# Performance work log

Measured on AMD Instinct MI355X. Metric: run time of the kernel, lower is better.

The kernel has to match this reference:

```python
import jax, jax.numpy as jnp
import numpy as np

K = 7          # kernel_size from init
PAD = (K - 1) // 2
EPS = 1e-8


def _local_std(x):
    """Per-pixel std of the zero-padded KxK x C neighborhood, matching
    torch: unfold(pad=3) -> mean over dim=1 (C*K*K) -> sqrt(mean(d^2)+eps).
    Computed with box-filter convolutions instead of materializing the
    49x-blown-up unfold tensor.
    Returns [B, H*W].
    """
    B, C, H, W = x.shape
    n = C * K * K  # fixed divisor (zero padding counts toward the mean)
    ones = jnp.ones((1, C, K, K), x.dtype)  # OIHW: sums over channels + window
    s = jax.lax.conv_general_dilated(x, ones, (1, 1), [(PAD, PAD), (PAD, PAD)])      # [B,1,H,W]
    s2 = jax.lax.conv_general_dilated(x * x, ones, (1, 1), [(PAD, PAD), (PAD, PAD)])  # [B,1,H,W]
    mu = s / n
    var = s2 / n - mu * mu  # E[x^2] - mu^2 == mean((x-mu)^2)
    return jnp.sqrt(var + EPS).reshape(B, H * W)


def _smooth_l1_mean(a, b):
    d = a - b
    ad = jnp.abs(d)
    per = jnp.where(ad < 1.0, 0.5 * d * d, ad - 0.5)
    return jnp.mean(per)


def setup_inputs() -> dict:
    key = jax.random.key(0)
    k1, k2 = jax.random.split(key)
    shape = (16, 3, 512, 512)
    pred_moire = jax.random.normal(k1, shape, dtype=jnp.float32)
    moire = jax.random.normal(k2, shape, dtype=jnp.float32)
    return {"pred_moire": pred_moire, "moire": moire}


def reference(pred_moire, moire):
    std_pred = _local_std(pred_moire)  # [B, H*W]
    std_tgt = _local_std(moire)        # [B, H*W]
    return _smooth_l1_mean(std_pred, std_tgt)  # scalar
```

## Files before the change

### kernel.cpp

```cpp
#include <hip/hip_runtime.h>


typedef float f32x4 __attribute__((ext_vector_type(4)));

#define K     7
#define PAD   3
#define TSX   64
#define TSY   32
#define HR    (TSY + K - 1)
#define LDSW  64
#define NT    256
#define NTASK (2 * HR * 8)

#define LOADQ(dst, ptr, OFF)                                        \
    asm volatile("global_load_dwordx4 %0, %1, off offset:" OFF      \
                 : "=v"(dst) : "v"(ptr))

#define WAITV(N) do {                                               \
    asm volatile("s_waitcnt vmcnt(" #N ")" ::: "memory");           \
    __builtin_amdgcn_sched_barrier(0);                              \
} while (0)

__global__ __launch_bounds__(NT, 2) void dist_loss_kernel(
    const float* __restrict__ pred,
    const float* __restrict__ tgt,
    float* __restrict__ out)
{
    constexpr int   C = 3, H = 512, W = 512;
    constexpr float INV_N     = 1.0f / (C * K * K);
    constexpr float INV_TOTAL = 1.0f / (16.0f * 512.0f * 512.0f);

    __shared__ float sh_s[2][HR][LDSW];
    __shared__ float sh_q[2][HR][LDSW];

    const int    tid  = threadIdx.x;
    const int    tx0  = blockIdx.x * TSX;
    const int    ty0  = blockIdx.y * TSY;
    const int    b    = blockIdx.z;
    const size_t plane = (size_t)H * W;

    const float* base0 = pred + (size_t)b * C * plane;
    const float* base1 = tgt  + (size_t)b * C * plane;

    float* shs = &sh_s[0][0][0];
    float* shq = &sh_q[0][0][0];

    #define DECL_SLOT(S)                                                     \
        const float *rB0_##S, *rB1_##S, *rB2_##S,                            \
                    *pA0_##S, *pA1_##S, *pA2_##S,                            \
                    *pE0_##S, *pE1_##S, *pE2_##S;                            \
        f32x4 qA0_##S, qB0_##S, qD0_##S, qE0_##S,                            \
              qA1_##S, qB1_##S, qD1_##S, qE1_##S,                            \
              qA2_##S, qB2_##S, qD2_##S, qE2_##S;                            \
        float m_##S, mL_##S, mR_##S; int idx_##S;

    #define SETUP(S, t) do {                                                 \
        const int which = ((t) >= HR * 8) ? 1 : 0;                           \
        const int tt    = (t) - which * (HR * 8);                            \
        const int row   = tt >> 3, cg = tt & 7;                              \
        const int gy    = ty0 - PAD + row;                                   \
        m_##S  = ((unsigned)gy < (unsigned)H) ? 1.f : 0.f;                   \
        const int gyc = min(max(gy, 0), H - 1);                              \
        const int gx0 = tx0 + (cg << 3);                                     \
        mL_##S = (gx0 > 0)   ? 1.f : 0.f;                                    \
        mR_##S = (gx0 < 504) ? 1.f : 0.f;                                    \
        const float* base = which ? base1 : base0;                           \
        rB0_##S = base + (size_t)gyc * W + gx0;                              \
        rB1_##S = rB0_##S + plane;                                           \
        rB2_##S = rB1_##S + plane;                                           \
        pA0_##S = rB0_##S + ((gx0 > 0)   ? -4 : 0);                          \
        pA1_##S = pA0_##S + plane;                                           \
        pA2_##S = pA1_##S + plane;                                           \
        pE0_##S = rB0_##S + ((gx0 < 504) ?  4 : 0);     \
        pE1_##S = pE0_##S + plane;                                           \
        pE2_##S = pE1_##S + plane;                                           \
        idx_##S = (which * HR + row) * LDSW + (cg << 3);                     \
    } while (0)

    #define ISSUE(S) do {                                                    \
        LOADQ(qA0_##S, pA0_##S, "0");  LOADQ(qB0_##S, rB0_##S, "0");         \
        LOADQ(qD0_##S, rB0_##S, "16"); LOADQ(qE0_##S, pE0_##S, "16");        \
        LOADQ(qA1_##S, pA1_##S, "0");  LOADQ(qB1_##S, rB1_##S, "0");         \
        LOADQ(qD1_##S, rB1_##S, "16"); LOADQ(qE1_##S, pE1_##S, "16");        \
        LOADQ(qA2_##S, pA2_##S, "0");  LOADQ(qB2_##S, rB2_##S, "0");         \
        LOADQ(qD2_##S, rB2_##S, "16"); LOADQ(qE2_##S, pE2_##S, "16");        \
    } while (0)

    #define CONSUME(S) do {                                                  \
        f32x4 tl = qA0_##S + qA1_##S + qA2_##S;                              \
        f32x4 ta = qB0_##S + qB1_##S + qB2_##S;                              \
        f32x4 tb = qD0_##S + qD1_##S + qD2_##S;                              \
        f32x4 tr = qE0_##S + qE1_##S + qE2_##S;                              \
        f32x4 ul = qA0_##S*qA0_##S + qA1_##S*qA1_##S + qA2_##S*qA2_##S;      \
        f32x4 ua = qB0_##S*qB0_##S + qB1_##S*qB1_##S + qB2_##S*qB2_##S;      \
        f32x4 ub = qD0_##S*qD0_##S + qD1_##S*qD1_##S + qD2_##S*qD2_##S;      \
        f32x4 ur = qE0_##S*qE0_##S + qE1_##S*qE1_##S + qE2_##S*qE2_##S;      \
        tl[1] *= mL_##S; tl[2] *= mL_##S; tl[3] *= mL_##S;                   \
        ul[1] *= mL_##S; ul[2] *= mL_##S; ul[3] *= mL_##S;                   \
        tr[0] *= mR_##S; tr[1] *= mR_##S; tr[2] *= mR_##S;                   \
        ur[0] *= mR_##S; ur[1] *= mR_##S; ur[2] *= mR_##S;                   \
        float h0 = tl[1]+tl[2]+tl[3]+ta[0]+ta[1]+ta[2]+ta[3];                \
        float h1 = h0 - tl[1] + tb[0];                                       \
        float h2 = h1 - tl[2] + tb[1];                                       \
        float h3 = h2 - tl[3] + tb[2];                                       \
        float h4 = h3 - ta[0] + tb[3];                                       \
        float h5 = h4 - ta[1] + tr[0];                                       \
        float h6 = h5 - ta[2] + tr[1];                                       \
        float h7 = h6 - ta[3] + tr[2];                                       \
        float g0 = ul[1]+ul[2]+ul[3]+ua[0]+ua[1]+ua[2]+ua[3];                \
        float g1 = g0 - ul[1] + ub[0];                                       \
        float g2 = g1 - ul[2] + ub[1];                                       \
        float g3 = g2 - ul[3] + ub[2];                                       \
        float g4 = g3 - ua[0] + ub[3];                                       \
        float g5 = g4 - ua[1] + ur[0];                                       \
        float g6 = g5 - ua[2] + ur[1];                                       \
        float g7 = g6 - ua[3] + ur[2];                                       \
        const float mm = m_##S;                                              \
        *(f32x4*)&shs[idx_##S]     = (f32x4){h0*mm, h1*mm, h2*mm, h3*mm};    \
        *(f32x4*)&shs[idx_##S + 4] = (f32x4){h4*mm, h5*mm, h6*mm, h7*mm};    \
        *(f32x4*)&shq[idx_##S]     = (f32x4){g0*mm, g1*mm, g2*mm, g3*mm};    \
        *(f32x4*)&shq[idx_##S + 4] = (f32x4){g4*mm, g5*mm, g6*mm, g7*mm};    \
    } while (0)

    DECL_SLOT(0);
    DECL_SLOT(1);
    const int t0 = tid;
    const int t1 = tid + NT;
    const int t2 = min(tid + 2 * NT, NTASK - 1);

    SETUP(0, t0); ISSUE(0);
    SETUP(1, t1); ISSUE(1);
    WAITV(12);
    CONSUME(0);
    SETUP(0, t2); ISSUE(0);
    WAITV(12);
    CONSUME(1);
    WAITV(0);
    CONSUME(0);

    __syncthreads();

    float acc = 0.0f;
    {
        const int rp = tid >> 4;
        const int x  = (tid & 15) << 2;

        f32x4 pA, pB;

        #define STD4(Sv, Qv, D) do {                                         \
            _Pragma("unroll")                                                \
            for (int c_ = 0; c_ < 4; ++c_) {                                 \
                float mu_ = (Sv)[c_] * INV_N;                                \
                (D)[c_] = sqrtf(fmaf(-mu_, mu_, (Qv)[c_] * INV_N) + 1e-8f);  \
            }                                                                \
        } while (0)
        #define SL1(a, bb) do {                                              \
            float d_  = (a) - (bb);                                          \
            float ad_ = fabsf(d_);                                           \
            acc += (ad_ < 1.0f) ? 0.5f * d_ * d_ : (ad_ - 0.5f);             \
        } while (0)

        #pragma unroll
        for (int w = 0; w < 2; ++w) {
            f32x4 S = (f32x4){0.f, 0.f, 0.f, 0.f};
            f32x4 Q = (f32x4){0.f, 0.f, 0.f, 0.f};
            #pragma unroll
            for (int k = 0; k < K; ++k) {
                S += *(const f32x4*)&sh_s[w][2 * rp + k][x];
                Q += *(const f32x4*)&sh_q[w][2 * rp + k][x];
            }
            f32x4 S2 = S - *(const f32x4*)&sh_s[w][2 * rp][x]
                         + *(const f32x4*)&sh_s[w][2 * rp + 7][x];
            f32x4 Q2 = Q - *(const f32x4*)&sh_q[w][2 * rp][x]
                         + *(const f32x4*)&sh_q[w][2 * rp + 7][x];

            if (w == 0) {
                STD4(S, Q, pA);
                STD4(S2, Q2, pB);
            } else {
                f32x4 sA, sB;
                STD4(S, Q, sA);
                STD4(S2, Q2, sB);
                SL1(pA[0], sA[0]); SL1(pA[1], sA[1]);
                SL1(pA[2], sA[2]); SL1(pA[3], sA[3]);
                SL1(pB[0], sB[0]); SL1(pB[1], sB[1]);
                SL1(pB[2], sB[2]); SL1(pB[3], sB[3]);
            }
        }
        #undef STD4
        #undef SL1
    }

    #pragma unroll
    for (int off = 32; off > 0; off >>= 1)
        acc += __shfl_down(acc, off, 64);

    __shared__ float wave_sums[NT / 64];
    if ((tid & 63) == 0) wave_sums[tid >> 6] = acc;
    __syncthreads();
    if (tid == 0) {
        float s = 0.0f;
        #pragma unroll
        for (int w = 0; w < NT / 64; ++w) s += wave_sums[w];
        atomicAdd(out, s * INV_TOTAL);
    }
}

extern "C" void kernel_launch(void* const* d_in, const int* in_sizes, int n_in,
                              void* d_out, int out_size, void* d_ws, size_t ws_size,
                              hipStream_t stream) {
    const float* pred = (const float*)d_in[0];
    const float* tgt  = (const float*)d_in[1];
    float* out = (float*)d_out;

    hipMemsetAsync(out, 0, sizeof(float), stream);

    dim3 grid(512 / TSX, 512 / TSY, 16);
    dist_loss_kernel<<<grid, NT, 0, stream>>>(pred, tgt, out);
}
```

Before: 130.2 us.

## Process four row tiles per block with double-buffered LDS and overlapped loads

Each block now walks four vertical tiles instead of one. It keeps three load slots in flight and prefetches the next tile's global loads while the current tile's vertical box-sum and loss phase runs out of a second LDS buffer. The intent is to hide global-memory latency behind compute and to cut the per-block launch and reduction overhead, since the grid shrinks fourfold. In exchange it uses more dynamic LDS (two buffers, near the two-blocks-per-CU limit) and more registers, and the grid becomes small enough to leave little slack for load balancing.

```diff
diff --git a/kernel.cpp b/kernel.cpp
--- a/kernel.cpp
+++ b/kernel.cpp
@@ -11,6 +11,7 @@
 #define LDSW  64
 #define NT    256
 #define NTASK (2 * HR * 8)
+#define NTILE 4
 
 #define LOADQ(dst, ptr, OFF)                                        \
     asm volatile("global_load_dwordx4 %0, %1, off offset:" OFF      \
@@ -30,60 +31,56 @@
     constexpr float INV_N     = 1.0f / (C * K * K);
     constexpr float INV_TOTAL = 1.0f / (16.0f * 512.0f * 512.0f);
 
-    __shared__ float sh_s[2][HR][LDSW];
-    __shared__ float sh_q[2][HR][LDSW];
+    extern __shared__ float smem[];
+    float* shs = smem;
+    float* shq = smem + 2 * 2 * HR * LDSW;
+    float* wave_sums = shq + 2 * 2 * HR * LDSW;
 
     const int    tid  = threadIdx.x;
     const int    tx0  = blockIdx.x * TSX;
-    const int    ty0  = blockIdx.y * TSY;
+    const int    tyb  = blockIdx.y * (NTILE * TSY);
     const int    b    = blockIdx.z;
     const size_t plane = (size_t)H * W;
 
     const float* base0 = pred + (size_t)b * C * plane;
     const float* base1 = tgt  + (size_t)b * C * plane;
 
-    float* shs = &sh_s[0][0][0];
-    float* shq = &sh_q[0][0][0];
+    const int rp = tid >> 4;
+    const int x  = (tid & 15) << 2;
 
     #define DECL_SLOT(S)                                                     \
-        const float *rB0_##S, *rB1_##S, *rB2_##S,                            \
-                    *pA0_##S, *pA1_##S, *pA2_##S,                            \
-                    *pE0_##S, *pE1_##S, *pE2_##S;                            \
         f32x4 qA0_##S, qB0_##S, qD0_##S, qE0_##S,                            \
               qA1_##S, qB1_##S, qD1_##S, qE1_##S,                            \
               qA2_##S, qB2_##S, qD2_##S, qE2_##S;                            \
         float m_##S, mL_##S, mR_##S; int idx_##S;
 
-    #define SETUP(S, t) do {                                                 \
+    #define SI(S, t, TY0, BUF) do {                                          \
         const int which = ((t) >= HR * 8) ? 1 : 0;                           \
         const int tt    = (t) - which * (HR * 8);                            \
         const int row   = tt >> 3, cg = tt & 7;                              \
-        const int gy    = ty0 - PAD + row;                                   \
+        const int gy    = (TY0) - PAD + row;                                 \
         m_##S  = ((unsigned)gy < (unsigned)H) ? 1.f : 0.f;                   \
         const int gyc = min(max(gy, 0), H - 1);                              \
         const int gx0 = tx0 + (cg << 3);                                     \
         mL_##S = (gx0 > 0)   ? 1.f : 0.f;                                    \
         mR_##S = (gx0 < 504) ? 1.f : 0.f;                                    \
         const float* base = which ? base1 : base0;                           \
-        rB0_##S = base + (size_t)gyc * W + gx0;                              \
-        rB1_##S = rB0_##S + plane;                                           \
-        rB2_##S = rB1_##S + plane;                                           \
-        pA0_##S = rB0_##S + ((gx0 > 0)   ? -4 : 0);                          \
-        pA1_##S = pA0_##S + plane;                                           \
-        pA2_##S = pA1_##S + plane;                                           \
-        pE0_##S = rB0_##S + ((gx0 < 504) ?  4 : 0);     \
-        pE1_##S = pE0_##S + plane;                                           \
-        pE2_##S = pE1_##S + plane;                                           \
-        idx_##S = (which * HR + row) * LDSW + (cg << 3);                     \
-    } while (0)
-
-    #define ISSUE(S) do {                                                    \
-        LOADQ(qA0_##S, pA0_##S, "0");  LOADQ(qB0_##S, rB0_##S, "0");         \
-        LOADQ(qD0_##S, rB0_##S, "16"); LOADQ(qE0_##S, pE0_##S, "16");        \
-        LOADQ(qA1_##S, pA1_##S, "0");  LOADQ(qB1_##S, rB1_##S, "0");         \
-        LOADQ(qD1_##S, rB1_##S, "16"); LOADQ(qE1_##S, pE1_##S, "16");        \
-        LOADQ(qA2_##S, pA2_##S, "0");  LOADQ(qB2_##S, rB2_##S, "0");         \
-        LOADQ(qD2_##S, rB2_##S, "16"); LOADQ(qE2_##S, pE2_##S, "16");        \
+        const float* rB0 = base + (size_t)gyc * W + gx0;                     \
+        const float* rB1 = rB0 + plane;                                      \
+        const float* rB2 = rB1 + plane;                                      \
+        const float* pA0 = rB0 + ((gx0 > 0)   ? -4 : 0);                     \
+        const float* pA1 = pA0 + plane;                                      \
+        const float* pA2 = pA1 + plane;                                      \
+        const float* pE0 = rB0 + ((gx0 < 504) ?  4 : 0);       \
+        const float* pE1 = pE0 + plane;                                      \
+        const float* pE2 = pE1 + plane;                                      \
+        idx_##S = (((BUF) * 2 + which) * HR + row) * LDSW + (cg << 3);       \
+        LOADQ(qA0_##S, pA0, "0");  LOADQ(qB0_##S, rB0, "0");                 \
+        LOADQ(qD0_##S, rB0, "16"); LOADQ(qE0_##S, pE0, "16");                \
+        LOADQ(qA1_##S, pA1, "0");  LOADQ(qB1_##S, rB1, "0");                 \
+        LOADQ(qD1_##S, rB1, "16"); LOADQ(qE1_##S, pE1, "16");                \
+        LOADQ(qA2_##S, pA2, "0");  LOADQ(qB2_##S, rB2, "0");                 \
+        LOADQ(qD2_##S, rB2, "16"); LOADQ(qE2_##S, pE2, "16");                \
     } while (0)
 
     #define CONSUME(S) do {                                                  \
@@ -122,80 +119,94 @@
         *(f32x4*)&shq[idx_##S + 4] = (f32x4){g4*mm, g5*mm, g6*mm, g7*mm};    \
     } while (0)
 
+    #define STD4(Sv, Qv, D) do {                                             \
+        _Pragma("unroll")                                                    \
+        for (int c_ = 0; c_ < 4; ++c_) {                                     \
+            float mu_ = (Sv)[c_] * INV_N;                                    \
+            (D)[c_] = sqrtf(fmaf(-mu_, mu_, (Qv)[c_] * INV_N) + 1e-8f);      \
+        }                                                                    \
+    } while (0)
+    #define SL1(a, bb) do {                                                  \
+        float d_  = (a) - (bb);                                              \
+        float ad_ = fabsf(d_);                                               \
+        acc += (ad_ < 1.0f) ? 0.5f * d_ * d_ : (ad_ - 0.5f);                 \
+    } while (0)
+
+    #define PHASE_B(BF) do {                                                 \
+        const float* bs_ = shs + (BF) * (2 * HR * LDSW);                     \
+        const float* bq_ = shq + (BF) * (2 * HR * LDSW);                     \
+        f32x4 pA, pB;                                                        \
+        _Pragma("unroll")                                                    \
+        for (int w = 0; w < 2; ++w) {                                        \
+            const float* rs_ = bs_ + w * (HR * LDSW);                        \
+            const float* rq_ = bq_ + w * (HR * LDSW);                        \
+            f32x4 S = (f32x4){0.f, 0.f, 0.f, 0.f};                           \
+            f32x4 Q = (f32x4){0.f, 0.f, 0.f, 0.f};                           \
+            _Pragma("unroll")                                                \
+            for (int k = 0; k < K; ++k) {                                    \
+                S += *(const f32x4*)&rs_[(2 * rp + k) * LDSW + x];           \
+                Q += *(const f32x4*)&rq_[(2 * rp + k) * LDSW + x];           \
+            }                                                                \
+            f32x4 S2 = S - *(const f32x4*)&rs_[(2 * rp) * LDSW + x]          \
+                         + *(const f32x4*)&rs_[(2 * rp + 7) * LDSW + x];     \
+            f32x4 Q2 = Q - *(const f32x4*)&rq_[(2 * rp) * LDSW + x]          \
+                         + *(const f32x4*)&rq_[(2 * rp + 7) * LDSW + x];     \
+            if (w == 0) {                                                    \
+                STD4(S, Q, pA);                                              \
+                STD4(S2, Q2, pB);                                            \
+            } else {                                                         \
+                f32x4 sA, sB;                                                \
+                STD4(S, Q, sA);                                              \
+                STD4(S2, Q2, sB);                                            \
+                SL1(pA[0], sA[0]); SL1(pA[1], sA[1]);                        \
+                SL1(pA[2], sA[2]); SL1(pA[3], sA[3]);                        \
+                SL1(pB[0], sB[0]); SL1(pB[1], sB[1]);                        \
+                SL1(pB[2], sB[2]); SL1(pB[3], sB[3]);                        \
+            }                                                                \
+        }                                                                    \
+    } while (0)
+
     DECL_SLOT(0);
     DECL_SLOT(1);
+    DECL_SLOT(2);
     const int t0 = tid;
     const int t1 = tid + NT;
     const int t2 = min(tid + 2 * NT, NTASK - 1);
 
-    SETUP(0, t0); ISSUE(0);
-    SETUP(1, t1); ISSUE(1);
-    WAITV(12);
-    CONSUME(0);
-    SETUP(0, t2); ISSUE(0);
-    WAITV(12);
-    CONSUME(1);
-    WAITV(0);
-    CONSUME(0);
-
+    float acc = 0.0f;
+
+    SI(0, t0, tyb, 0);
+    SI(1, t1, tyb, 0);
+    SI(2, t2, tyb, 0);
+
+    #pragma unroll
+    for (int n = 0; n < NTILE - 1; ++n) {
+        const int tyn = tyb + (n + 1) * TSY;
+        const int pn  = (n + 1) & 1;
+        WAITV(24); CONSUME(0); SI(0, t0, tyn, pn);
+        WAITV(24); CONSUME(1); SI(1, t1, tyn, pn);
+        WAITV(24); CONSUME(2); SI(2, t2, tyn, pn);
+        __syncthreads();
+        PHASE_B(n & 1);
+    }
+
+    WAITV(24); CONSUME(0);
+    WAITV(12); CONSUME(1);
+    WAITV(0);  CONSUME(2);
     __syncthreads();
-
-    float acc = 0.0f;
-    {
-        const int rp = tid >> 4;
-        const int x  = (tid & 15) << 2;
-
-        f32x4 pA, pB;
-
-        #define STD4(Sv, Qv, D) do {                                         \
-            _Pragma("unroll")                                                \
-            for (int c_ = 0; c_ < 4; ++c_) {                                 \
-                float mu_ = (Sv)[c_] * INV_N;                                \
-                (D)[c_] = sqrtf(fmaf(-mu_, mu_, (Qv)[c_] * INV_N) + 1e-8f);  \
-            }                                                                \
-        } while (0)
-        #define SL1(a, bb) do {                                              \
-            float d_  = (a) - (bb);                                          \
-            float ad_ = fabsf(d_);                                           \
-            acc += (ad_ < 1.0f) ? 0.5f * d_ * d_ : (ad_ - 0.5f);             \
-        } while (0)
-
-        #pragma unroll
-        for (int w = 0; w < 2; ++w) {
-            f32x4 S = (f32x4){0.f, 0.f, 0.f, 0.f};
-            f32x4 Q = (f32x4){0.f, 0.f, 0.f, 0.f};
-            #pragma unroll
-            for (int k = 0; k < K; ++k) {
-                S += *(const f32x4*)&sh_s[w][2 * rp + k][x];
-                Q += *(const f32x4*)&sh_q[w][2 * rp + k][x];
-            }
-            f32x4 S2 = S - *(const f32x4*)&sh_s[w][2 * rp][x]
-                         + *(const f32x4*)&sh_s[w][2 * rp + 7][x];
-            f32x4 Q2 = Q - *(const f32x4*)&sh_q[w][2 * rp][x]
-                         + *(const f32x4*)&sh_q[w][2 * rp + 7][x];
-
-            if (w == 0) {
-                STD4(S, Q, pA);
-                STD4(S2, Q2, pB);
-            } else {
-                f32x4 sA, sB;
-                STD4(S, Q, sA);
-                STD4(S2, Q2, sB);
-                SL1(pA[0], sA[0]); SL1(pA[1], sA[1]);
-                SL1(pA[2], sA[2]); SL1(pA[3], sA[3]);
-                SL1(pB[0], sB[0]); SL1(pB[1], sB[1]);
-                SL1(pB[2], sB[2]); SL1(pB[3], sB[3]);
-            }
-        }
-        #undef STD4
-        #undef SL1
-    }
+    PHASE_B((NTILE - 1) & 1);
+
+    #undef SI
+    #undef CONSUME
+    #undef PHASE_B
+    #undef STD4
+    #undef SL1
 
     #pragma unroll
     for (int off = 32; off > 0; off >>= 1)
         acc += __shfl_down(acc, off, 64);
 
-    __shared__ float wave_sums[NT / 64];
+    __syncthreads();
     if ((tid & 63) == 0) wave_sums[tid >> 6] = acc;
     __syncthreads();
     if (tid == 0) {
@@ -215,6 +226,8 @@
 
     hipMemsetAsync(out, 0, sizeof(float), stream);
 
-    dim3 grid(512 / TSX, 512 / TSY, 16);
-    dist_loss_kernel<<<grid, NT, 0, stream>>>(pred, tgt, out);
+    const size_t lds_bytes = (2 * 2 * HR * LDSW * 2 + 4) * sizeof(float);
+
+    dim3 grid(512 / TSX, 512 / (TSY * NTILE), 16);
+    dist_loss_kernel<<<grid, NT, lds_bytes, stream>>>(pred, tgt, out);
 }
```

New measurement: 128.5 us. Within noise of the previous version (-1.3%).
